# Performance work log

Measured on AMD Instinct MI355X. Metric: run time of the kernel, lower is better.

## Reference

```python
import jax, jax.numpy as jnp
import numpy as np


def _expm_batch(S):
    # S: [..., m, m] skew-symmetric -> elementwise matrix exponential
    flat = S.reshape((-1,) + S.shape[-2:])
    E = jax.vmap(jax.scipy.linalg.expm)(flat)
    return E.reshape(S.shape)


def _time_prod(M):
    # M: [B, T, m, m] -> Z = M[:,T-1] @ ... @ M[:,0]  (dyadic, log-depth, matches DevNet dyadic_prod order)
    B, T, m, _ = M.shape
    eye = jnp.eye(m, dtype=M.dtype)
    while M.shape[1] > 1:
        if M.shape[1] % 2 == 1:
            pad = jnp.broadcast_to(eye, (B, 1, m, m))
            M = jnp.concatenate([M, pad], axis=1)
        # later factor on the left: M[:,1::2] @ M[:,0::2]
        M = jnp.einsum('btij,btjk->btik', M[:, 1::2], M[:, 0::2])
    return M[:, 0]


def setup_inputs() -> dict:
    key = jax.random.key(0)
    k1, k2, k3 = jax.random.split(key, 3)
    B, T, Cin, m, O = 64, 2048, 8, 16, 10
    X = jax.random.normal(k1, (B, T, Cin), dtype=jnp.float32)
    A = jax.random.normal(k2, (m, m, Cin), dtype=jnp.float32) * 0.2
    W = jax.random.normal(k3, (O, m * m), dtype=jnp.float32) * (1.0 / np.sqrt(m * m))
    b = jnp.zeros((O,), dtype=jnp.float32)
    return {"X": X, "A": A, "W": W, "b": b}


def reference(X, A, W, b):
    # skew-symmetric parametrization of the Lie algebra so(m)
    A_skew = A - jnp.swapaxes(A, 0, 1)          # [m, m, Cin]
    dX = X[:, 1:] - X[:, :-1]                    # [B, T-1, Cin] path increments
    S = jnp.einsum('btc,ijc->btij', dX, A_skew)  # [B, T-1, m, m] skew per step
    M = _expm_batch(S)                           # per-step SO(m) elements
    Z = _time_prod(M)                            # [B, m, m] path development
    out = Z.reshape(Z.shape[0], -1) @ W.T + b    # [B, n_outputs]
    return out
```

## Files before the change

### kernel.cpp

```cpp
#include <hip/hip_runtime.h>

#define BSZ   64
#define TLEN  2048
#define NSTEP 2047
#define CIN   8
#define NCH   128
#define CHL   16
#define TSTR  20

typedef __attribute__((ext_vector_type(4))) float        fx4;
typedef __attribute__((ext_vector_type(4))) _Float16     hx4;
typedef __attribute__((ext_vector_type(2))) unsigned int ux2;
typedef __attribute__((ext_vector_type(4))) unsigned int ux4;

__device__ __forceinline__ void splitf(const fx4 v, hx4& hi, hx4& lo) {
    _Float16 h0 = (_Float16)v[0], h1 = (_Float16)v[1];
    _Float16 h2 = (_Float16)v[2], h3 = (_Float16)v[3];
    hi[0] = h0; hi[1] = h1; hi[2] = h2; hi[3] = h3;
    lo[0] = (_Float16)(v[0] - (float)h0);
    lo[1] = (_Float16)(v[1] - (float)h1);
    lo[2] = (_Float16)(v[2] - (float)h2);
    lo[3] = (_Float16)(v[3] - (float)h3);
}

__device__ __forceinline__ fx4 mm3(hx4 ah, hx4 al, hx4 bh, hx4 bl) {
    fx4 acc = {0.f, 0.f, 0.f, 0.f};
    acc = __builtin_amdgcn_mfma_f32_16x16x16f16(ah, bh, acc, 0, 0, 0);
    acc = __builtin_amdgcn_mfma_f32_16x16x16f16(ah, bl, acc, 0, 0, 0);
    acc = __builtin_amdgcn_mfma_f32_16x16x16f16(al, bh, acc, 0, 0, 0);
    return acc;
}

__device__ __forceinline__ fx4 ldsT(float* ts, int m, int c, fx4 v) {
    ts[(4 * m + 0) * TSTR + c] = v[0];
    ts[(4 * m + 1) * TSTR + c] = v[1];
    ts[(4 * m + 2) * TSTR + c] = v[2];
    ts[(4 * m + 3) * TSTR + c] = v[3];
    return *(const fx4*)&ts[c * TSTR + 4 * m];
}

__device__ __forceinline__ void ldsT_h(unsigned* tsu, int m, int c,
                                       hx4 Bh, hx4 Bl, hx4& Ah, hx4& Al) {
    ux2 bh = __builtin_bit_cast(ux2, Bh);
    ux2 bl = __builtin_bit_cast(ux2, Bl);
    unsigned w0 = (bh[0] & 0xFFFFu) | (bl[0] << 16);
    unsigned w1 = (bh[0] >> 16)     | (bl[0] & 0xFFFF0000u);
    unsigned w2 = (bh[1] & 0xFFFFu) | (bl[1] << 16);
    unsigned w3 = (bh[1] >> 16)     | (bl[1] & 0xFFFF0000u);
    tsu[(4 * m + 0) * TSTR + c] = w0;
    tsu[(4 * m + 1) * TSTR + c] = w1;
    tsu[(4 * m + 2) * TSTR + c] = w2;
    tsu[(4 * m + 3) * TSTR + c] = w3;
    ux4 rd = *(const ux4*)&tsu[c * TSTR + 4 * m];
    ux2 ah, al;
    ah[0] = (rd[0] & 0xFFFFu) | (rd[1] << 16);
    al[0] = (rd[0] >> 16)     | (rd[1] & 0xFFFF0000u);
    ah[1] = (rd[2] & 0xFFFFu) | (rd[3] << 16);
    al[1] = (rd[2] >> 16)     | (rd[3] & 0xFFFF0000u);
    Ah = __builtin_bit_cast(hx4, ah);
    Al = __builtin_bit_cast(hx4, al);
}

__global__ __launch_bounds__(256)
void devnet_expm_chunk(const float* __restrict__ X, const float* __restrict__ A,
                       float* __restrict__ G)
{
    __shared__ __align__(16) unsigned Ts[4][16 * TSTR];

    const int tid  = threadIdx.x;
    const int wid  = tid >> 6;
    const int lane = tid & 63;
    const int m    = lane >> 4;
    const int c    = lane & 15;
    const int gw   = blockIdx.x * 4 + wid;
    const int b    = gw >> 7;
    const int ch   = gw & (NCH - 1);
    unsigned* tsu = Ts[wid];
    float*    tsf = (float*)Ts[wid];

    float ask[4][CIN];
#pragma unroll
    for (int r = 0; r < 4; ++r) {
        const int i = 4 * m + r;
#pragma unroll
        for (int cc = 0; cc < CIN; ++cc)
            ask[r][cc] = A[(i * 16 + c) * CIN + cc] - A[(c * 16 + i) * CIN + cc];
    }

    fx4 idv;
#pragma unroll
    for (int r = 0; r < 4; ++r) idv[r] = (4 * m + r == c) ? 1.f : 0.f;

    fx4 P = idv;

    const int t0 = ch * CHL;
    const int t1 = (t0 + CHL < NSTEP) ? (t0 + CHL) : NSTEP;

    for (int t = t0; t < t1; ++t) {
        const float* xp = X + ((size_t)b * TLEN + t) * CIN;
        const float4 x0 = *reinterpret_cast<const float4*>(xp + 0);
        const float4 x1 = *reinterpret_cast<const float4*>(xp + 4);
        const float4 y0 = *reinterpret_cast<const float4*>(xp + 8);
        const float4 y1 = *reinterpret_cast<const float4*>(xp + 12);
        float dx[CIN];
        dx[0] = y0.x - x0.x; dx[1] = y0.y - x0.y; dx[2] = y0.z - x0.z; dx[3] = y0.w - x0.w;
        dx[4] = y1.x - x1.x; dx[5] = y1.y - x1.y; dx[6] = y1.z - x1.z; dx[7] = y1.w - x1.w;

        fx4 sv;
#pragma unroll
        for (int r = 0; r < 4; ++r) {
            float acc = 0.f;
#pragma unroll
            for (int cc = 0; cc < CIN; ++cc) acc = fmaf(dx[cc], ask[r][cc], acc);
            sv[r] = acc;
        }

        float a = fabsf(sv[0]) + fabsf(sv[1]) + fabsf(sv[2]) + fabsf(sv[3]);
        a += __shfl_xor(a, 16, 64);
        a += __shfl_xor(a, 32, 64);
        a = fmaxf(a, __shfl_xor(a, 1, 64));
        a = fmaxf(a, __shfl_xor(a, 2, 64));
        a = fmaxf(a, __shfl_xor(a, 4, 64));
        a = fmaxf(a, __shfl_xor(a, 8, 64));

        int e;
        (void)frexpf(a, &e);
        int sc = e + 2;
        if (sc < 0) sc = 0;
        const float scale = ldexpf(1.0f, -sc);

        fx4 xv = sv * scale;
        fx4 nxv = -xv;
        hx4 Xah, Xal;
        splitf(nxv, Xah, Xal);

        fx4 R = idv + xv * 0.2f;
#pragma unroll
        for (int k = 4; k >= 1; --k) {
            hx4 Rh, Rl;
            splitf(R, Rh, Rl);
            fx4 acc = mm3(Xah, Xal, Rh, Rl);
            R = idv + acc * (1.f / (float)k);
        }

        for (int q = 0; q < sc; ++q) {
            hx4 Bh, Bl, Ah, Al;
            splitf(R, Bh, Bl);
            ldsT_h(tsu, m, c, Bh, Bl, Ah, Al);
            R = mm3(Ah, Al, Bh, Bl);
        }

        {
            fx4 Ra = ldsT(tsf, m, c, R);
            hx4 Ah, Al, Ph, Pl;
            splitf(Ra, Ah, Al);
            splitf(P, Ph, Pl);
            P = mm3(Ah, Al, Ph, Pl);
        }
    }

    *reinterpret_cast<fx4*>(G + ((size_t)b * NCH + ch) * 256 + lane * 4) = P;
}

__global__ __launch_bounds__(64)
void devnet_reduce1(float* __restrict__ G)
{
    __shared__ __align__(16) float Ts[16 * TSTR];

    const int lane = threadIdx.x;
    const int m    = lane >> 4;
    const int c    = lane & 15;
    const int b    = blockIdx.x >> 2;
    const int w    = blockIdx.x & 3;

    float* base = G + ((size_t)b * NCH + w * 32) * 256;

    fx4 Acc = *reinterpret_cast<const fx4*>(base + lane * 4);
    for (int cc = 1; cc < 32; ++cc) {
        fx4 Q  = *reinterpret_cast<const fx4*>(base + (size_t)cc * 256 + lane * 4);
        fx4 Qa = ldsT(Ts, m, c, Q);
        hx4 Ah, Al, Bh, Bl;
        splitf(Qa, Ah, Al);
        splitf(Acc, Bh, Bl);
        Acc = mm3(Ah, Al, Bh, Bl);
    }
    *reinterpret_cast<fx4*>(base + lane * 4) = Acc;
}

__global__ __launch_bounds__(64)
void devnet_reduce2(const float* __restrict__ G, const float* __restrict__ W,
                    const float* __restrict__ bias, float* __restrict__ out)
{
    __shared__ __align__(16) float Ts[16 * TSTR];
    __shared__ float Zf[256];

    const int lane = threadIdx.x;
    const int m    = lane >> 4;
    const int c    = lane & 15;
    const int b    = blockIdx.x;

    const float* gb = G + (size_t)b * NCH * 256;

    fx4 Acc = *reinterpret_cast<const fx4*>(gb + lane * 4);
    for (int w = 1; w < 4; ++w) {
        fx4 Q  = *reinterpret_cast<const fx4*>(gb + (size_t)(w * 32) * 256 + lane * 4);
        fx4 Qa = ldsT(Ts, m, c, Q);
        hx4 Ah, Al, Bh, Bl;
        splitf(Qa, Ah, Al);
        splitf(Acc, Bh, Bl);
        Acc = mm3(Ah, Al, Bh, Bl);
    }
#pragma unroll
    for (int r = 0; r < 4; ++r) Zf[(4 * m + r) * 16 + c] = Acc[r];

    for (int o = 0; o < 10; ++o) {
        const float* wo = W + o * 256;
        float v = Zf[lane] * wo[lane];
        v = fmaf(Zf[lane + 64],  wo[lane + 64],  v);
        v = fmaf(Zf[lane + 128], wo[lane + 128], v);
        v = fmaf(Zf[lane + 192], wo[lane + 192], v);
#pragma unroll
        for (int off = 32; off >= 1; off >>= 1) v += __shfl_down(v, off, 64);
        if (lane == 0) out[b * 10 + o] = v + bias[o];
    }
}

extern "C" void kernel_launch(void* const* d_in, const int* in_sizes, int n_in,
                              void* d_out, int out_size, void* d_ws, size_t ws_size,
                              hipStream_t stream)
{
    const float* X    = (const float*)d_in[0];
    const float* A    = (const float*)d_in[1];
    const float* W    = (const float*)d_in[2];
    const float* bias = (const float*)d_in[3];
    float* out = (float*)d_out;
    float* G   = (float*)d_ws;

    devnet_expm_chunk<<<BSZ * NCH / 4, 256, 0, stream>>>(X, A, G);
    devnet_reduce1<<<BSZ * 4, 64, 0, stream>>>(G);
    devnet_reduce2<<<BSZ, 64, 0, stream>>>(G, W, bias, out);
}
```

Measured before the change: 194.5 us.

## Replace LDS transposes with identity-MFMA transposes and rebalance chunk reduction

Drops the shared-memory transpose round-trips in the expm, squaring and accumulation steps. Each transpose is now done in registers by multiplying the hi/lo fp16 halves by an identity matrix with MFMA, and the results are packed with cvt_pkrtz. The first reduction is reshaped from 4 groups of 32 chunks to 16 groups of 8 (256-thread blocks), and the second reduction now chains 16 partials instead of 4. This removes LDS traffic and waits from the serial chain, at the cost of two extra MFMAs per transpose and round-toward-zero packing of the transposed values.

Result: no change. 195.4 us (+0.4%).

```diff
diff --git a/kernel.cpp b/kernel.cpp
--- a/kernel.cpp
+++ b/kernel.cpp
@@ -6,21 +6,22 @@
 #define CIN   8
 #define NCH   128
 #define CHL   16
-#define TSTR  20
-
-typedef __attribute__((ext_vector_type(4))) float        fx4;
-typedef __attribute__((ext_vector_type(4))) _Float16     hx4;
-typedef __attribute__((ext_vector_type(2))) unsigned int ux2;
-typedef __attribute__((ext_vector_type(4))) unsigned int ux4;
+
+typedef __attribute__((ext_vector_type(4))) float    fx4;
+typedef __attribute__((ext_vector_type(4))) _Float16 hx4;
+
+__device__ __forceinline__ hx4 pk4(float a, float b, float c, float d) {
+    auto p0 = __builtin_amdgcn_cvt_pkrtz(a, b);
+    auto p1 = __builtin_amdgcn_cvt_pkrtz(c, d);
+    hx4 r; r[0] = p0[0]; r[1] = p0[1]; r[2] = p1[0]; r[3] = p1[1];
+    return r;
+}
 
 __device__ __forceinline__ void splitf(const fx4 v, hx4& hi, hx4& lo) {
     _Float16 h0 = (_Float16)v[0], h1 = (_Float16)v[1];
     _Float16 h2 = (_Float16)v[2], h3 = (_Float16)v[3];
     hi[0] = h0; hi[1] = h1; hi[2] = h2; hi[3] = h3;
-    lo[0] = (_Float16)(v[0] - (float)h0);
-    lo[1] = (_Float16)(v[1] - (float)h1);
-    lo[2] = (_Float16)(v[2] - (float)h2);
-    lo[3] = (_Float16)(v[3] - (float)h3);
+    lo = pk4(v[0] - (float)h0, v[1] - (float)h1, v[2] - (float)h2, v[3] - (float)h3);
 }
 
 __device__ __forceinline__ fx4 mm3(hx4 ah, hx4 al, hx4 bh, hx4 bl) {
@@ -31,42 +32,18 @@
     return acc;
 }
 
-__device__ __forceinline__ fx4 ldsT(float* ts, int m, int c, fx4 v) {
-    ts[(4 * m + 0) * TSTR + c] = v[0];
-    ts[(4 * m + 1) * TSTR + c] = v[1];
-    ts[(4 * m + 2) * TSTR + c] = v[2];
-    ts[(4 * m + 3) * TSTR + c] = v[3];
-    return *(const fx4*)&ts[c * TSTR + 4 * m];
-}
-
-__device__ __forceinline__ void ldsT_h(unsigned* tsu, int m, int c,
-                                       hx4 Bh, hx4 Bl, hx4& Ah, hx4& Al) {
-    ux2 bh = __builtin_bit_cast(ux2, Bh);
-    ux2 bl = __builtin_bit_cast(ux2, Bl);
-    unsigned w0 = (bh[0] & 0xFFFFu) | (bl[0] << 16);
-    unsigned w1 = (bh[0] >> 16)     | (bl[0] & 0xFFFF0000u);
-    unsigned w2 = (bh[1] & 0xFFFFu) | (bl[1] << 16);
-    unsigned w3 = (bh[1] >> 16)     | (bl[1] & 0xFFFF0000u);
-    tsu[(4 * m + 0) * TSTR + c] = w0;
-    tsu[(4 * m + 1) * TSTR + c] = w1;
-    tsu[(4 * m + 2) * TSTR + c] = w2;
-    tsu[(4 * m + 3) * TSTR + c] = w3;
-    ux4 rd = *(const ux4*)&tsu[c * TSTR + 4 * m];
-    ux2 ah, al;
-    ah[0] = (rd[0] & 0xFFFFu) | (rd[1] << 16);
-    al[0] = (rd[0] >> 16)     | (rd[1] & 0xFFFF0000u);
-    ah[1] = (rd[2] & 0xFFFFu) | (rd[3] << 16);
-    al[1] = (rd[2] >> 16)     | (rd[3] & 0xFFFF0000u);
-    Ah = __builtin_bit_cast(hx4, ah);
-    Al = __builtin_bit_cast(hx4, al);
+__device__ __forceinline__ void mfmaT(hx4 Mh, hx4 Ml, hx4 Ih, hx4& Th, hx4& Tl) {
+    fx4 z = {0.f, 0.f, 0.f, 0.f};
+    fx4 th = __builtin_amdgcn_mfma_f32_16x16x16f16(Mh, Ih, z, 0, 0, 0);
+    fx4 tl = __builtin_amdgcn_mfma_f32_16x16x16f16(Ml, Ih, z, 0, 0, 0);
+    Th = pk4(th[0], th[1], th[2], th[3]);
+    Tl = pk4(tl[0], tl[1], tl[2], tl[3]);
 }
 
 __global__ __launch_bounds__(256)
 void devnet_expm_chunk(const float* __restrict__ X, const float* __restrict__ A,
                        float* __restrict__ G)
 {
-    __shared__ __align__(16) unsigned Ts[4][16 * TSTR];
-
     const int tid  = threadIdx.x;
     const int wid  = tid >> 6;
     const int lane = tid & 63;
@@ -75,8 +52,6 @@
     const int gw   = blockIdx.x * 4 + wid;
     const int b    = gw >> 7;
     const int ch   = gw & (NCH - 1);
-    unsigned* tsu = Ts[wid];
-    float*    tsf = (float*)Ts[wid];
 
     float ask[4][CIN];
 #pragma unroll
@@ -90,6 +65,7 @@
     fx4 idv;
 #pragma unroll
     for (int r = 0; r < 4; ++r) idv[r] = (4 * m + r == c) ? 1.f : 0.f;
+    const hx4 Ih = pk4(idv[0], idv[1], idv[2], idv[3]);
 
     fx4 P = idv;
 
@@ -134,55 +110,65 @@
         hx4 Xah, Xal;
         splitf(nxv, Xah, Xal);
 
-        fx4 R = idv + xv * 0.2f;
+        fx4 R;
+#pragma unroll
+        for (int r = 0; r < 4; ++r) R[r] = fmaf(xv[r], 0.2f, idv[r]);
 #pragma unroll
         for (int k = 4; k >= 1; --k) {
             hx4 Rh, Rl;
             splitf(R, Rh, Rl);
             fx4 acc = mm3(Xah, Xal, Rh, Rl);
-            R = idv + acc * (1.f / (float)k);
+            const float inv = 1.f / (float)k;
+#pragma unroll
+            for (int r = 0; r < 4; ++r) R[r] = fmaf(acc[r], inv, idv[r]);
         }
 
         for (int q = 0; q < sc; ++q) {
-            hx4 Bh, Bl, Ah, Al;
-            splitf(R, Bh, Bl);
-            ldsT_h(tsu, m, c, Bh, Bl, Ah, Al);
-            R = mm3(Ah, Al, Bh, Bl);
+            hx4 Rh, Rl, Th, Tl;
+            splitf(R, Rh, Rl);
+            mfmaT(Rh, Rl, Ih, Th, Tl);
+            R = mm3(Th, Tl, Rh, Rl);
         }
 
         {
-            fx4 Ra = ldsT(tsf, m, c, R);
-            hx4 Ah, Al, Ph, Pl;
-            splitf(Ra, Ah, Al);
+            hx4 Rh, Rl, Th, Tl, Ph, Pl;
+            splitf(R, Rh, Rl);
+            mfmaT(Rh, Rl, Ih, Th, Tl);
             splitf(P, Ph, Pl);
-            P = mm3(Ah, Al, Ph, Pl);
+            P = mm3(Th, Tl, Ph, Pl);
         }
     }
 
     *reinterpret_cast<fx4*>(G + ((size_t)b * NCH + ch) * 256 + lane * 4) = P;
 }
 
-__global__ __launch_bounds__(64)
+__global__ __launch_bounds__(256)
 void devnet_reduce1(float* __restrict__ G)
 {
-    __shared__ __align__(16) float Ts[16 * TSTR];
-
-    const int lane = threadIdx.x;
+    const int tid  = threadIdx.x;
+    const int wid  = tid >> 6;
+    const int lane = tid & 63;
     const int m    = lane >> 4;
     const int c    = lane & 15;
-    const int b    = blockIdx.x >> 2;
-    const int w    = blockIdx.x & 3;
-
-    float* base = G + ((size_t)b * NCH + w * 32) * 256;
+    const int gw   = blockIdx.x * 4 + wid;
+    const int b    = gw >> 4;
+    const int w    = gw & 15;
+
+    fx4 idv;
+#pragma unroll
+    for (int r = 0; r < 4; ++r) idv[r] = (4 * m + r == c) ? 1.f : 0.f;
+    const hx4 Ih = pk4(idv[0], idv[1], idv[2], idv[3]);
+
+    float* base = G + ((size_t)b * NCH + w * 8) * 256;
 
     fx4 Acc = *reinterpret_cast<const fx4*>(base + lane * 4);
-    for (int cc = 1; cc < 32; ++cc) {
-        fx4 Q  = *reinterpret_cast<const fx4*>(base + (size_t)cc * 256 + lane * 4);
-        fx4 Qa = ldsT(Ts, m, c, Q);
-        hx4 Ah, Al, Bh, Bl;
-        splitf(Qa, Ah, Al);
+    for (int cc = 1; cc < 8; ++cc) {
+        fx4 Q = *reinterpret_cast<const fx4*>(base + (size_t)cc * 256 + lane * 4);
+        hx4 Qh, Ql, Th, Tl, Bh, Bl;
+        splitf(Q, Qh, Ql);
+        mfmaT(Qh, Ql, Ih, Th, Tl);
         splitf(Acc, Bh, Bl);
-        Acc = mm3(Ah, Al, Bh, Bl);
+        Acc = mm3(Th, Tl, Bh, Bl);
     }
     *reinterpret_cast<fx4*>(base + lane * 4) = Acc;
 }
@@ -191,7 +177,6 @@
 void devnet_reduce2(const float* __restrict__ G, const float* __restrict__ W,
                     const float* __restrict__ bias, float* __restrict__ out)
 {
-    __shared__ __align__(16) float Ts[16 * TSTR];
     __shared__ float Zf[256];
 
     const int lane = threadIdx.x;
@@ -199,17 +184,23 @@
     const int c    = lane & 15;
     const int b    = blockIdx.x;
 
+    fx4 idv;
+#pragma unroll
+    for (int r = 0; r < 4; ++r) idv[r] = (4 * m + r == c) ? 1.f : 0.f;
+    const hx4 Ih = pk4(idv[0], idv[1], idv[2], idv[3]);
+
     const float* gb = G + (size_t)b * NCH * 256;
 
     fx4 Acc = *reinterpret_cast<const fx4*>(gb + lane * 4);
-    for (int w = 1; w < 4; ++w) {
-        fx4 Q  = *reinterpret_cast<const fx4*>(gb + (size_t)(w * 32) * 256 + lane * 4);
-        fx4 Qa = ldsT(Ts, m, c, Q);
-        hx4 Ah, Al, Bh, Bl;
-        splitf(Qa, Ah, Al);
+    for (int k = 1; k < 16; ++k) {
+        fx4 Q = *reinterpret_cast<const fx4*>(gb + (size_t)(k * 8) * 256 + lane * 4);
+        hx4 Qh, Ql, Th, Tl, Bh, Bl;
+        splitf(Q, Qh, Ql);
+        mfmaT(Qh, Ql, Ih, Th, Tl);
         splitf(Acc, Bh, Bl);
-        Acc = mm3(Ah, Al, Bh, Bl);
-    }
+        Acc = mm3(Th, Tl, Bh, Bl);
+    }
+
 #pragma unroll
     for (int r = 0; r < 4; ++r) Zf[(4 * m + r) * 16 + c] = Acc[r];
 
@@ -237,6 +228,6 @@
     float* G   = (float*)d_ws;
 
     devnet_expm_chunk<<<BSZ * NCH / 4, 256, 0, stream>>>(X, A, G);
-    devnet_reduce1<<<BSZ * 4, 64, 0, stream>>>(G);
+    devnet_reduce1<<<BSZ * 16 / 4, 256, 0, stream>>>(G);
     devnet_reduce2<<<BSZ, 64, 0, stream>>>(G, W, bias, out);
 }
```
